# Performance work log

Hardware: AMD Instinct MI355X
Metric: run time of the kernel (lower is better)

Reference implementation:

```python
import jax, jax.numpy as jnp
import numpy as np

PLACEHOLDER = -1
B, S, V = 128, 8, 32000  # batch, spec tokens per request, vocab
T = B * S


def setup_inputs() -> dict:
    key = jax.random.key(0)
    ks = jax.random.split(key, 8)
    target_logits = jax.random.normal(ks[0], (T, V), dtype=jnp.float32)
    dp = jax.random.uniform(ks[1], (T, V), dtype=jnp.float32)
    draft_probs = dp / jnp.sum(dp, axis=-1, keepdims=True)  # valid prob dist per token
    draft_token_ids = jax.random.randint(ks[2], (T,), 0, V, dtype=jnp.int32)
    bonus_token_ids = jax.random.randint(ks[3], (B,), 0, V, dtype=jnp.int32)
    temperature = 0.5 + jax.random.uniform(ks[4], (B,), dtype=jnp.float32)  # >0 => all random
    uniform_probs = jax.random.uniform(ks[5], (T,), dtype=jnp.float32)
    # q ~ Exponential(1), as torch's q.exponential_()
    u = jax.random.uniform(ks[6], (B, V), dtype=jnp.float32, minval=1e-10, maxval=1.0)
    q = -jnp.log(u)
    cu_num_draft_tokens = (jnp.arange(B, dtype=jnp.int32) + 1) * S
    return {
        'target_logits': target_logits,
        'draft_probs': draft_probs,
        'draft_token_ids': draft_token_ids,
        'bonus_token_ids': bonus_token_ids,
        'temperature': temperature,
        'uniform_probs': uniform_probs,
        'q': q,
        'cu_num_draft_tokens': cu_num_draft_tokens,
    }


def reference(target_logits, draft_probs, draft_token_ids, bonus_token_ids,
              temperature, uniform_probs, q, cu_num_draft_tokens):
    # compute_probs: softmax of logits / per-token expanded temperature
    temp_tok = jnp.repeat(temperature, S)  # [T]
    target_probs = jax.nn.softmax(target_logits / temp_tok[:, None], axis=-1)  # [T, V]

    tok = jnp.arange(T)
    req = tok // S  # request index per token (uniform raggedness)

    # accept/reject: target_prob/draft_prob >= u  (guard draft_prob > 0)
    p_tgt = target_probs[tok, draft_token_ids]  # [T]
    p_drf = draft_probs[tok, draft_token_ids]   # [T]
    accept = (p_drf > 0) & (p_tgt >= uniform_probs * p_drf)  # [T]

    # recovered tokens: argmax(max(p_tgt - p_drf, 0) / q) over vocab (Gumbel-max trick)
    resid = jnp.maximum(target_probs - draft_probs, 0.0)  # [T, V]
    recovered = jnp.argmax(resid / q[req], axis=-1).astype(jnp.int32)  # [T]

    # sequential accept until first rejection, then placeholder; bonus if all accepted
    accept_b = accept.reshape(B, S)
    alive = jnp.concatenate(
        [jnp.ones((B, 1), dtype=bool),
         jnp.cumprod(accept_b[:, :-1].astype(jnp.int32), axis=1).astype(bool)],
        axis=1)  # alive[b, p] = all accepts before pos p
    tok_out = jnp.where(accept_b, draft_token_ids.reshape(B, S), recovered.reshape(B, S))
    main = jnp.where(alive, tok_out, PLACEHOLDER)  # [B, S]
    all_acc = jnp.all(accept_b, axis=1)
    bonus_col = jnp.where(all_acc, bonus_token_ids, PLACEHOLDER)  # [B]
    output_token_ids = jnp.concatenate([main, bonus_col[:, None]], axis=1)  # [B, S+1]
    return output_token_ids
```

## Files before the change

### kernel.cpp

```cpp
#include <hip/hip_runtime.h>


constexpr int PLACEHOLDER = -1;
constexpr int B = 128;
constexpr int S = 8;
constexpr int V = 32000;
constexpr int T = B * S;
constexpr int NV4 = V / 4;
constexpr int HV4 = NV4 / 2;

extern "C" __device__ float __builtin_amdgcn_exp2f(float);
extern "C" __device__ float __builtin_amdgcn_rcpf(float);

__global__ __launch_bounds__(512)
void k1_sum(const float* __restrict__ logits,
            const float* __restrict__ dprobs,
            const int*   __restrict__ draft_ids,
            const float* __restrict__ temperature,
            const float* __restrict__ uniform_probs,
            float* __restrict__ w_D,
            int*   __restrict__ w_acc,
            int*   __restrict__ w_flag)
{
    const int t   = blockIdx.x;
    const int tid = threadIdx.x, lane = tid & 63, wid = tid >> 6;
    __shared__ float s_red[8];

    if (tid == 0 && t < B) w_flag[t] = 0;

    const float c = 1.4426950408889634f / temperature[t >> 3];
    const float4* lrow = (const float4*)(logits + (size_t)t * V);

    int dt = 0; float l_d = 0.f, d_d = 0.f, u = 0.f;
    if (tid == 0) {
        dt  = draft_ids[t];
        l_d = logits[(size_t)t * V + dt];
        d_d = dprobs[(size_t)t * V + dt];
        u   = uniform_probs[t];
    }

    float lsum = 0.f;
    #pragma unroll 4
    for (int j = 0; j < 16; ++j) {
        const int i4 = j * 512 + tid;
        if (i4 < NV4) {
            const float4 v = lrow[i4];
            lsum += (__builtin_amdgcn_exp2f(v.x * c) +
                     __builtin_amdgcn_exp2f(v.y * c)) +
                    (__builtin_amdgcn_exp2f(v.z * c) +
                     __builtin_amdgcn_exp2f(v.w * c));
        }
    }
    #pragma unroll
    for (int off = 32; off >= 1; off >>= 1)
        lsum += __shfl_xor(lsum, off, 64);
    if (lane == 0) s_red[wid] = lsum;
    __syncthreads();
    if (tid == 0) {
        const float D = ((s_red[0] + s_red[1]) + (s_red[2] + s_red[3])) +
                        ((s_red[4] + s_red[5]) + (s_red[6] + s_red[7]));
        w_D[t] = D;
        const float e_d = __builtin_amdgcn_exp2f(l_d * c);
        w_acc[t] = (d_d > 0.f) && (e_d >= u * d_d * D);
    }
}

__global__ __launch_bounds__(512)
void k2_arg(const float* __restrict__ logits,
            const float* __restrict__ dprobs,
            const float* __restrict__ q,
            const float* __restrict__ temperature,
            const float* __restrict__ w_D,
            const int*   __restrict__ w_acc,
            const int*   __restrict__ draft_ids,
            const int*   __restrict__ bonus_ids,
            float* __restrict__ w_hbv,
            int*   __restrict__ w_hbi,
            int*   __restrict__ w_flag,
            int*   __restrict__ out)
{
    const int bid = blockIdx.x;
    const int b = bid >> 1, h = bid & 1;
    const int tid = threadIdx.x, lane = tid & 63, wid = tid >> 6;
    __shared__ float s_val[8];
    __shared__ int   s_idx[8];
    __shared__ int   s_needp;

    if (tid == 0) {
        int np = S;
        #pragma unroll
        for (int p = S - 1; p >= 0; --p)
            if (!w_acc[b * S + p]) np = p;
        s_needp = np;
    }
    __syncthreads();
    const int need_p = s_needp;
    if (need_p >= S) {
        if (h == 0 && tid == 0) {
            #pragma unroll
            for (int p = 0; p < S; ++p)
                out[b * (S + 1) + p] = draft_ids[b * S + p];
            out[b * (S + 1) + S] = bonus_ids[b];
        }
        return;
    }

    const int   t = b * S + need_p;
    const float c = 1.4426950408889634f / temperature[b];
    const float D = w_D[t];

    const float4* lrow = (const float4*)(logits + (size_t)t * V) + h * HV4;
    const float4* drow = (const float4*)(dprobs + (size_t)t * V) + h * HV4;
    const float4* qrow = (const float4*)(q      + (size_t)b * V) + h * HV4;

    float bestv = -__builtin_inff();
    int   besti = 0x7fffffff;

#define RS_COMP(LC, DC, QC, GIDX)                                          \
    {                                                                      \
        const float e  = __builtin_amdgcn_exp2f((LC) * c);                 \
        const float rq = __builtin_amdgcn_rcpf(QC);                        \
        const float r  = fmaf(-((DC) * rq), D, e * rq);                    \
        if (r > bestv) { bestv = r; besti = (GIDX); }                      \
    }

    #pragma unroll
    for (int ph = 0; ph < 2; ++ph) {
        float4 lv[4], dv[4], qv[4];
        #pragma unroll
        for (int j = 0; j < 4; ++j) {
            const int i = (ph * 4 + j) * 512 + tid;
            if (i < HV4) lv[j] = lrow[i];
        }
        #pragma unroll
        for (int j = 0; j < 4; ++j) {
            const int i = (ph * 4 + j) * 512 + tid;
            if (i < HV4) dv[j] = drow[i];
        }
        #pragma unroll
        for (int j = 0; j < 4; ++j) {
            const int i = (ph * 4 + j) * 512 + tid;
            if (i < HV4) qv[j] = qrow[i];
        }
        #pragma unroll
        for (int j = 0; j < 4; ++j) {
            const int i = (ph * 4 + j) * 512 + tid;
            if (i < HV4) {
                const int base = (h * HV4 + i) * 4;
                RS_COMP(lv[j].x, dv[j].x, qv[j].x, base + 0)
                RS_COMP(lv[j].y, dv[j].y, qv[j].y, base + 1)
                RS_COMP(lv[j].z, dv[j].z, qv[j].z, base + 2)
                RS_COMP(lv[j].w, dv[j].w, qv[j].w, base + 3)
            }
        }
    }
#undef RS_COMP

    #pragma unroll
    for (int off = 32; off >= 1; off >>= 1) {
        const float ov = __shfl_xor(bestv, off, 64);
        const int   oi = __shfl_xor(besti, off, 64);
        if (ov > bestv || (ov == bestv && oi < besti)) { bestv = ov; besti = oi; }
    }
    if (lane == 0) { s_val[wid] = bestv; s_idx[wid] = besti; }
    __syncthreads();

    if (tid == 0) {
        float bv = s_val[0]; int bi = s_idx[0];
        #pragma unroll
        for (int w = 1; w < 8; ++w) {
            const float ov = s_val[w]; const int oi = s_idx[w];
            if (ov > bv || (ov == bv && oi < bi)) { bv = ov; bi = oi; }
        }
        if (h == 1) {
            __hip_atomic_store(&w_hbv[b], bv, __ATOMIC_RELAXED,
                               __HIP_MEMORY_SCOPE_AGENT);
            __hip_atomic_store(&w_hbi[b], bi, __ATOMIC_RELAXED,
                               __HIP_MEMORY_SCOPE_AGENT);
            asm volatile("s_waitcnt vmcnt(0)" ::: "memory");
            __hip_atomic_store(&w_flag[b], 1, __ATOMIC_RELAXED,
                               __HIP_MEMORY_SCOPE_AGENT);
        } else {
            while (__hip_atomic_load(&w_flag[b], __ATOMIC_RELAXED,
                                     __HIP_MEMORY_SCOPE_AGENT) == 0)
                __builtin_amdgcn_s_sleep(2);
            const float pbv = __hip_atomic_load(&w_hbv[b], __ATOMIC_RELAXED,
                                                __HIP_MEMORY_SCOPE_AGENT);
            const int   pbi = __hip_atomic_load(&w_hbi[b], __ATOMIC_RELAXED,
                                                __HIP_MEMORY_SCOPE_AGENT);
            if (pbv > bv) { bv = pbv; bi = pbi; }
            #pragma unroll
            for (int p = 0; p < S; ++p) {
                int tok = PLACEHOLDER;
                if (p < need_p)       tok = draft_ids[b * S + p];
                else if (p == need_p) tok = bi;
                out[b * (S + 1) + p] = tok;
            }
            out[b * (S + 1) + S] = PLACEHOLDER;
        }
    }
}

extern "C" void kernel_launch(void* const* d_in, const int* in_sizes, int n_in,
                              void* d_out, int out_size, void* d_ws, size_t ws_size,
                              hipStream_t stream) {
    const float* logits      = (const float*)d_in[0];
    const float* dprobs      = (const float*)d_in[1];
    const int*   draft_ids   = (const int*)d_in[2];
    const int*   bonus_ids   = (const int*)d_in[3];
    const float* temperature = (const float*)d_in[4];
    const float* uniform     = (const float*)d_in[5];
    const float* q           = (const float*)d_in[6];

    int* out = (int*)d_out;
    float* w_D    = (float*)d_ws;
    int*   w_acc  = (int*)(w_D + T);
    float* w_hbv  = (float*)(w_acc + T);
    int*   w_hbi  = (int*)(w_hbv + B);
    int*   w_flag = w_hbi + B;

    k1_sum<<<T, 512, 0, stream>>>(logits, dprobs, draft_ids, temperature,
                                  uniform, w_D, w_acc, w_flag);
    k2_arg<<<2 * B, 512, 0, stream>>>(logits, dprobs, q, temperature,
                                      w_D, w_acc, draft_ids, bonus_ids,
                                      w_hbv, w_hbi, w_flag, out);
}
```

Before: 36.46 us.

## Fuse softmax-sum and residual-argmax kernels with inter-block sequence-flag sync

Merges the two kernels into one launch. Every block first computes its token's softmax denominator and accept bit and publishes them with a per-token sequence value. The blocks at positions 0 and 4 of each request then spin until all eight tokens of that request are published, and do the two-half residual argmax. This removes the second launch and the gap between kernels. The risks are spin-wait stalls and deadlock if blocks are not co-resident in launch order. The sequence values are also constant and never reset, so a repeated call can read the previous call's published data before it is overwritten.

```diff
diff --git a/kernel.cpp b/kernel.cpp
--- a/kernel.cpp
+++ b/kernel.cpp
@@ -12,86 +12,100 @@
 extern "C" __device__ float __builtin_amdgcn_exp2f(float);
 extern "C" __device__ float __builtin_amdgcn_rcpf(float);
 
-__global__ __launch_bounds__(512)
-void k1_sum(const float* __restrict__ logits,
+__device__ __forceinline__ unsigned long long seq1(int t) {
+    return 0xC0FFEE5500000000ull + (unsigned int)t;
+}
+__device__ __forceinline__ unsigned long long seq2(int b) {
+    return 0xBEEF77AA00000000ull + (unsigned int)b;
+}
+
+__global__ __launch_bounds__(512, 4)
+void rs_all(const float* __restrict__ logits,
             const float* __restrict__ dprobs,
+            const float* __restrict__ q,
             const int*   __restrict__ draft_ids,
+            const int*   __restrict__ bonus_ids,
             const float* __restrict__ temperature,
             const float* __restrict__ uniform_probs,
+            unsigned long long* __restrict__ w_seq,
+            unsigned long long* __restrict__ w_pseq,
             float* __restrict__ w_D,
             int*   __restrict__ w_acc,
-            int*   __restrict__ w_flag)
+            float* __restrict__ w_hbv,
+            int*   __restrict__ w_hbi,
+            int*   __restrict__ out)
 {
     const int t   = blockIdx.x;
+    const int b   = t >> 3;
     const int tid = threadIdx.x, lane = tid & 63, wid = tid >> 6;
     __shared__ float s_red[8];
-
-    if (tid == 0 && t < B) w_flag[t] = 0;
-
-    const float c = 1.4426950408889634f / temperature[t >> 3];
-    const float4* lrow = (const float4*)(logits + (size_t)t * V);
-
-    int dt = 0; float l_d = 0.f, d_d = 0.f, u = 0.f;
-    if (tid == 0) {
-        dt  = draft_ids[t];
-        l_d = logits[(size_t)t * V + dt];
-        d_d = dprobs[(size_t)t * V + dt];
-        u   = uniform_probs[t];
-    }
-
-    float lsum = 0.f;
-    #pragma unroll 4
-    for (int j = 0; j < 16; ++j) {
-        const int i4 = j * 512 + tid;
-        if (i4 < NV4) {
-            const float4 v = lrow[i4];
-            lsum += (__builtin_amdgcn_exp2f(v.x * c) +
-                     __builtin_amdgcn_exp2f(v.y * c)) +
-                    (__builtin_amdgcn_exp2f(v.z * c) +
-                     __builtin_amdgcn_exp2f(v.w * c));
-        }
-    }
-    #pragma unroll
-    for (int off = 32; off >= 1; off >>= 1)
-        lsum += __shfl_xor(lsum, off, 64);
-    if (lane == 0) s_red[wid] = lsum;
-    __syncthreads();
-    if (tid == 0) {
-        const float D = ((s_red[0] + s_red[1]) + (s_red[2] + s_red[3])) +
-                        ((s_red[4] + s_red[5]) + (s_red[6] + s_red[7]));
-        w_D[t] = D;
-        const float e_d = __builtin_amdgcn_exp2f(l_d * c);
-        w_acc[t] = (d_d > 0.f) && (e_d >= u * d_d * D);
-    }
-}
-
-__global__ __launch_bounds__(512)
-void k2_arg(const float* __restrict__ logits,
-            const float* __restrict__ dprobs,
-            const float* __restrict__ q,
-            const float* __restrict__ temperature,
-            const float* __restrict__ w_D,
-            const int*   __restrict__ w_acc,
-            const int*   __restrict__ draft_ids,
-            const int*   __restrict__ bonus_ids,
-            float* __restrict__ w_hbv,
-            int*   __restrict__ w_hbi,
-            int*   __restrict__ w_flag,
-            int*   __restrict__ out)
-{
-    const int bid = blockIdx.x;
-    const int b = bid >> 1, h = bid & 1;
-    const int tid = threadIdx.x, lane = tid & 63, wid = tid >> 6;
     __shared__ float s_val[8];
     __shared__ int   s_idx[8];
     __shared__ int   s_needp;
+    __shared__ float s_D2;
+
+    const float c = 1.4426950408889634f / temperature[b];
+
+    {
+        const float4* lrow = (const float4*)(logits + (size_t)t * V);
+        int dt = 0; float l_d = 0.f, d_d = 0.f, u = 0.f;
+        if (tid == 0) {
+            dt  = draft_ids[t];
+            l_d = logits[(size_t)t * V + dt];
+            d_d = dprobs[(size_t)t * V + dt];
+            u   = uniform_probs[t];
+        }
+        float lsum = 0.f;
+        #pragma unroll 4
+        for (int j = 0; j < 16; ++j) {
+            const int i4 = j * 512 + tid;
+            if (i4 < NV4) {
+                const float4 v = lrow[i4];
+                lsum += (__builtin_amdgcn_exp2f(v.x * c) +
+                         __builtin_amdgcn_exp2f(v.y * c)) +
+                        (__builtin_amdgcn_exp2f(v.z * c) +
+                         __builtin_amdgcn_exp2f(v.w * c));
+            }
+        }
+        #pragma unroll
+        for (int off = 32; off >= 1; off >>= 1)
+            lsum += __shfl_xor(lsum, off, 64);
+        if (lane == 0) s_red[wid] = lsum;
+        __syncthreads();
+        if (tid == 0) {
+            const float D = ((s_red[0] + s_red[1]) + (s_red[2] + s_red[3])) +
+                            ((s_red[4] + s_red[5]) + (s_red[6] + s_red[7]));
+            __hip_atomic_store(&w_D[t], D, __ATOMIC_RELAXED,
+                               __HIP_MEMORY_SCOPE_AGENT);
+            const float e_d = __builtin_amdgcn_exp2f(l_d * c);
+            const int acc = (d_d > 0.f) && (e_d >= u * d_d * D);
+            __hip_atomic_store(&w_acc[t], acc, __ATOMIC_RELAXED,
+                               __HIP_MEMORY_SCOPE_AGENT);
+            asm volatile("s_waitcnt vmcnt(0)" ::: "memory");
+            __hip_atomic_store(&w_seq[t], seq1(t), __ATOMIC_RELAXED,
+                               __HIP_MEMORY_SCOPE_AGENT);
+        }
+    }
+
+    const int role = t & 7;
+    if (role != 0 && role != 4) return;
+    const int h = (role == 4);
 
     if (tid == 0) {
+        for (int p = 0; p < S; ++p) {
+            const int tp = b * S + p;
+            while (__hip_atomic_load(&w_seq[tp], __ATOMIC_RELAXED,
+                                     __HIP_MEMORY_SCOPE_AGENT) != seq1(tp))
+                __builtin_amdgcn_s_sleep(4);
+        }
         int np = S;
-        #pragma unroll
         for (int p = S - 1; p >= 0; --p)
-            if (!w_acc[b * S + p]) np = p;
+            if (!__hip_atomic_load(&w_acc[b * S + p], __ATOMIC_RELAXED,
+                                   __HIP_MEMORY_SCOPE_AGENT)) np = p;
         s_needp = np;
+        if (np < S)
+            s_D2 = __hip_atomic_load(&w_D[b * S + np], __ATOMIC_RELAXED,
+                                     __HIP_MEMORY_SCOPE_AGENT);
     }
     __syncthreads();
     const int need_p = s_needp;
@@ -105,13 +119,12 @@
         return;
     }
 
-    const int   t = b * S + need_p;
-    const float c = 1.4426950408889634f / temperature[b];
-    const float D = w_D[t];
-
-    const float4* lrow = (const float4*)(logits + (size_t)t * V) + h * HV4;
-    const float4* drow = (const float4*)(dprobs + (size_t)t * V) + h * HV4;
-    const float4* qrow = (const float4*)(q      + (size_t)b * V) + h * HV4;
+    const int   tt = b * S + need_p;
+    const float D  = s_D2;
+
+    const float4* lrow = (const float4*)(logits + (size_t)tt * V) + h * HV4;
+    const float4* drow = (const float4*)(dprobs + (size_t)tt * V) + h * HV4;
+    const float4* qrow = (const float4*)(q      + (size_t)b  * V) + h * HV4;
 
     float bestv = -__builtin_inff();
     int   besti = 0x7fffffff;
@@ -178,12 +191,12 @@
             __hip_atomic_store(&w_hbi[b], bi, __ATOMIC_RELAXED,
                                __HIP_MEMORY_SCOPE_AGENT);
             asm volatile("s_waitcnt vmcnt(0)" ::: "memory");
-            __hip_atomic_store(&w_flag[b], 1, __ATOMIC_RELAXED,
+            __hip_atomic_store(&w_pseq[b], seq2(b), __ATOMIC_RELAXED,
                                __HIP_MEMORY_SCOPE_AGENT);
         } else {
-            while (__hip_atomic_load(&w_flag[b], __ATOMIC_RELAXED,
-                                     __HIP_MEMORY_SCOPE_AGENT) == 0)
-                __builtin_amdgcn_s_sleep(2);
+            while (__hip_atomic_load(&w_pseq[b], __ATOMIC_RELAXED,
+                                     __HIP_MEMORY_SCOPE_AGENT) != seq2(b))
+                __builtin_amdgcn_s_sleep(4);
             const float pbv = __hip_atomic_load(&w_hbv[b], __ATOMIC_RELAXED,
                                                 __HIP_MEMORY_SCOPE_AGENT);
             const int   pbi = __hip_atomic_load(&w_hbi[b], __ATOMIC_RELAXED,
@@ -213,15 +226,14 @@
     const float* q           = (const float*)d_in[6];
 
     int* out = (int*)d_out;
-    float* w_D    = (float*)d_ws;
-    int*   w_acc  = (int*)(w_D + T);
-    float* w_hbv  = (float*)(w_acc + T);
-    int*   w_hbi  = (int*)(w_hbv + B);
-    int*   w_flag = w_hbi + B;
-
-    k1_sum<<<T, 512, 0, stream>>>(logits, dprobs, draft_ids, temperature,
-                                  uniform, w_D, w_acc, w_flag);
-    k2_arg<<<2 * B, 512, 0, stream>>>(logits, dprobs, q, temperature,
-                                      w_D, w_acc, draft_ids, bonus_ids,
-                                      w_hbv, w_hbi, w_flag, out);
-}
+    unsigned long long* w_seq  = (unsigned long long*)d_ws;
+    unsigned long long* w_pseq = w_seq + T;
+    float* w_D   = (float*)(w_pseq + B);
+    int*   w_acc = (int*)(w_D + T);
+    float* w_hbv = (float*)(w_acc + T);
+    int*   w_hbi = (int*)(w_hbv + B);
+
+    rs_all<<<T, 512, 0, stream>>>(logits, dprobs, q, draft_ids, bonus_ids,
+                                  temperature, uniform,
+                                  w_seq, w_pseq, w_D, w_acc, w_hbv, w_hbi, out);
+}
```

After: 48.77 us. +33.8%, slower.
